# Optimization experiments

Measured on AMD Instinct MI355X. Metric: run time of the kernel, lower is better.

## Reference

```python
import jax, jax.numpy as jnp
import numpy as np

B, T, HW = 16, 64, 7
D = 768          # input_dim == base_dim
N = 12           # num_heads
C = D // N       # head_dim = 64
EPS = 1e-5


def layernorm(x, g, b):
    m = jnp.mean(x, axis=-1, keepdims=True)
    v = jnp.mean((x - m) ** 2, axis=-1, keepdims=True)
    return (x - m) * jax.lax.rsqrt(v + EPS) * g + b


def setup_inputs() -> dict:
    key = jax.random.key(0)
    ks = jax.random.split(key, 12)
    s = lambda k, shape: (jax.random.normal(k, shape, jnp.float32) * 0.02)
    return {
        "x": jax.random.normal(ks[0], (B, T, HW, HW, D), jnp.float32),
        "W_qkv": s(ks[1], (D, 3 * D)),                  # qkv_bias=False
        "Wpq": s(ks[2], (C, C, HW, HW)), "bpq": jnp.zeros((C,), jnp.float32),
        "Wpk": s(ks[3], (C, C, HW, HW)), "bpk": jnp.zeros((C,), jnp.float32),
        "Wpv": s(ks[4], (C, C, HW, HW)), "bpv": jnp.zeros((C,), jnp.float32),
        "g_q": jnp.ones((C,), jnp.float32), "be_q": jnp.zeros((C,), jnp.float32),
        "g_k": jnp.ones((C,), jnp.float32), "be_k": jnp.zeros((C,), jnp.float32),
        "g_v": jnp.ones((C,), jnp.float32), "be_v": jnp.zeros((C,), jnp.float32),
        "rel_pos_t": s(ks[5], (2 * T - 1, C)),          # (127, 64): matches dt, no interp
        "W_proj": s(ks[6], (D, D)), "b_proj": jnp.zeros((D,), jnp.float32),
    }


def reference(x, W_qkv, Wpq, bpq, Wpk, bpk, Wpv, bpv,
              g_q, be_q, g_k, be_k, g_v, be_v, rel_pos_t, W_proj, b_proj):
    b, t = x.shape[0], x.shape[1]
    # qkv projection -> (B,T,H,W,3,N,C)
    qkv = (x @ W_qkv).reshape(b, t, HW, HW, 3, N, C)
    q3, k3, v3 = qkv[..., 0, :, :], qkv[..., 1, :, :], qkv[..., 2, :, :]  # (B,T,H,W,N,C)
    # Conv3d kernel (1,7,7) on full 7x7 spatial == contraction over (h,w,c_in)
    q = jnp.einsum('bthwnc,dchw->bntd', q3, Wpq) + bpq   # (B,N,T,C)
    k = jnp.einsum('bthwnc,dchw->bntd', k3, Wpk) + bpk
    v = jnp.einsum('bthwnc,dchw->bntd', v3, Wpv) + bpv
    q = layernorm(q, g_q, be_q)
    k = layernorm(k, g_k, be_k)
    v = layernorm(v, g_v, be_v)
    scale = C ** -0.5
    attn = jnp.einsum('bntc,bnsc->bnts', q * scale, k)   # (B,N,T,T)
    # relative temporal position bias: gather table rows by distance, matmul with q
    dist = jnp.arange(t)[:, None] - jnp.arange(t)[None, :] + (t - 1)  # (T,T) in [0,2T-2]
    Rt = rel_pos_t[dist]                                  # (T,T,C)
    rel = jnp.einsum('bntc,tsc->bnts', q, Rt)
    attn = jax.nn.softmax(attn + rel, axis=-1)
    out = jnp.einsum('bnts,bnsc->bntc', attn, v) + q      # residual add of q
    out = out.transpose(0, 2, 1, 3).reshape(b, t, N * C)  # (B,T,D)
    return out @ W_proj + b_proj
```

## Files before the change

### kernel.cpp

```cpp
#include <hip/hip_runtime.h>


typedef __attribute__((ext_vector_type(8))) short bf16x8;
typedef __attribute__((ext_vector_type(4))) float f32x4;

#define AS1U(p) ((const __attribute__((address_space(1))) unsigned int*)(p))
#define AS3U(p) ((__attribute__((address_space(3))) unsigned int*)(p))

__device__ __forceinline__ unsigned short cvt_bf16(float x) {
  union { float f; unsigned int u; } v; v.f = x;
  unsigned int r = v.u + 0x7fffu + ((v.u >> 16) & 1u);
  return (unsigned short)(r >> 16);
}
__device__ __forceinline__ float bf2f(unsigned short h) {
  union { unsigned int u; float f; } v; v.u = ((unsigned int)h) << 16;
  return v.f;
}

__device__ __forceinline__ void wg_barrier() {
  asm volatile("" ::: "memory");
  __builtin_amdgcn_s_barrier();
  asm volatile("" ::: "memory");
}

__global__ __launch_bounds__(256) void cvt_x_k(const float* __restrict__ src,
                                               unsigned short* __restrict__ dst, int n8) {
  int i = blockIdx.x * 256 + threadIdx.x;
  if (i >= n8) return;
  const float4* s = (const float4*)src + (size_t)i * 2;
  float4 a = s[0], b = s[1];
  ushort4 r0 = { cvt_bf16(a.x), cvt_bf16(a.y), cvt_bf16(a.z), cvt_bf16(a.w) };
  ushort4 r1 = { cvt_bf16(b.x), cvt_bf16(b.y), cvt_bf16(b.z), cvt_bf16(b.w) };
  ushort4* d = (ushort4*)dst + (size_t)i * 2;
  d[0] = r0; d[1] = r1;
}

__global__ __launch_bounds__(256) void transpose_cvt_k(const float* __restrict__ src,
                                                       unsigned short* __restrict__ dst) {
  __shared__ float tl[32][33];
  int k0 = blockIdx.x * 32, n0 = blockIdx.y * 32;
  int tx = threadIdx.x & 31, ty = threadIdx.x >> 5;
#pragma unroll
  for (int r = 0; r < 32; r += 8)
    tl[ty + r][tx] = src[(size_t)(k0 + ty + r) * 2304 + n0 + tx];
  __syncthreads();
#pragma unroll
  for (int r = 0; r < 32; r += 8)
    dst[(size_t)(n0 + ty + r) * 768 + k0 + tx] = cvt_bf16(tl[tx][ty + r]);
}

__global__ __launch_bounds__(256) void prep_cvt_k(
    const float* __restrict__ Wpq, const float* __restrict__ Wpk,
    const float* __restrict__ Wpv, const float* __restrict__ relp,
    unsigned short* __restrict__ WpTT, unsigned short* __restrict__ relb) {
  int bid = blockIdx.x;
  if (bid < 2400) {
    int p = bid / 800;
    const float* src = (p == 0) ? Wpq : (p == 1) ? Wpk : Wpv;
    unsigned short* dst = WpTT + (size_t)p * 204800;
    int o = (bid - p * 800) * 256 + threadIdx.x;
    if (o >= 204800) return;
    int c = o & 63, d = (o >> 6) & 63, hw = o >> 12;
    dst[o] = (hw < 49) ? cvt_bf16(src[d * 3136 + c * 49 + hw]) : (unsigned short)0;
  } else {
    int i = (bid - 2400) * 256 + threadIdx.x;
    relb[i] = (i < 8128) ? cvt_bf16(relp[i]) : (unsigned short)0;
  }
}

__global__ __launch_bounds__(256, 2) void gemm_qkv_128(
    const unsigned short* __restrict__ A, const unsigned short* __restrict__ Bt,
    unsigned short* __restrict__ Cb, int nb_off) {
  __shared__ unsigned short As[2][8192];
  __shared__ unsigned short Bs[2][8192];

  const int orig = blockIdx.x;
  const int xcd = orig & 7;
  const int slot = orig >> 3;
  const int mb = xcd * 49 + slot / 9;
  const int nb = slot % 9 + nb_off;
  const int m0 = mb * 128, n0 = nb * 128;
  const int K = 768;

  const int tid = threadIdx.x;
  const int wave = tid >> 6, lane = tid & 63;
  const int quad = lane >> 4, l16 = lane & 15;
  const int wr = wave >> 1, wc = wave & 1;
  const int x7 = l16 & 7;

  const int srow = tid >> 3;
  const int cs = (tid & 7) ^ (srow & 7);
  const unsigned short* Ag[4];
  const unsigned short* Bg[4];
#pragma unroll
  for (int l = 0; l < 4; ++l) {
    Ag[l] = A + (size_t)(m0 + l * 32 + srow) * K + cs * 8;
    Bg[l] = Bt + (size_t)(n0 + l * 32 + srow) * K + cs * 8;
  }
  const int ldst = wave * 512;

#define STAGE_A(buf, kt) do {                                                      \
    const int ko_ = (kt) * 64;                                                     \
    _Pragma("unroll")                                                              \
    for (int l_ = 0; l_ < 4; ++l_)                                                 \
      __builtin_amdgcn_global_load_lds(AS1U(Ag[l_] + ko_),                         \
          AS3U(&As[buf][l_ * 2048 + ldst]), 16, 0, 0);                             \
  } while (0)

#define STAGE_B(buf, kt) do {                                                      \
    const int ko_ = (kt) * 64;                                                     \
    _Pragma("unroll")                                                              \
    for (int l_ = 0; l_ < 4; ++l_)                                                 \
      __builtin_amdgcn_global_load_lds(AS1U(Bg[l_] + ko_),                         \
          AS3U(&Bs[buf][l_ * 2048 + ldst]), 16, 0, 0);                             \
  } while (0)

#define LDA(dst, buf, mi) do {                                                     \
    _Pragma("unroll")                                                              \
    for (int fi_ = 0; fi_ < 2; ++fi_) {                                            \
      const int row_ = wr * 64 + (mi) * 32 + fi_ * 16 + l16;                       \
      _Pragma("unroll")                                                            \
      for (int ks_ = 0; ks_ < 2; ++ks_)                                            \
        dst[fi_][ks_] = *(const bf16x8*)&As[buf][row_ * 64 +                       \
            (((ks_ * 4 + quad) ^ x7) * 8)];                                        \
    }                                                                              \
  } while (0)

#define LDB(dst, buf, nj) do {                                                     \
    _Pragma("unroll")                                                              \
    for (int fj_ = 0; fj_ < 2; ++fj_) {                                            \
      const int row_ = wc * 64 + (nj) * 32 + fj_ * 16 + l16;                       \
      _Pragma("unroll")                                                            \
      for (int ks_ = 0; ks_ < 2; ++ks_)                                            \
        dst[fj_][ks_] = *(const bf16x8*)&Bs[buf][row_ * 64 +                       \
            (((ks_ * 4 + quad) ^ x7) * 8)];                                        \
    }                                                                              \
  } while (0)

#define MFMAQ(a_, b_, mi, nj) do {                                                 \
    _Pragma("unroll")                                                              \
    for (int ks_ = 0; ks_ < 2; ++ks_)                                              \
      _Pragma("unroll")                                                            \
      for (int fi_ = 0; fi_ < 2; ++fi_)                                            \
        _Pragma("unroll")                                                          \
        for (int fj_ = 0; fj_ < 2; ++fj_)                                          \
          acc[(mi) * 2 + fi_][(nj) * 2 + fj_] =                                    \
              __builtin_amdgcn_mfma_f32_16x16x32_bf16(a_[fi_][ks_],                \
                  b_[fj_][ks_], acc[(mi) * 2 + fi_][(nj) * 2 + fj_], 0, 0, 0);     \
  } while (0)

#define ITER(cur, DO_STAGE, kt2, VMI) do {                                         \
    asm volatile("s_waitcnt vmcnt(" #VMI ")" ::: "memory");                        \
    wg_barrier();                                                                  \
                                                           \
    LDA(af0, cur, 0); LDB(bf0, cur, 0);                                            \
    wg_barrier();                                                                  \
    __builtin_amdgcn_s_setprio(1); MFMAQ(af0, bf0, 0, 0);                          \
    __builtin_amdgcn_s_setprio(0);                                                 \
    wg_barrier();                                                                  \
                                                           \
    LDB(bf1, cur, 1);                                                              \
    wg_barrier();                                                                  \
    __builtin_amdgcn_s_setprio(1); MFMAQ(af0, bf1, 0, 1);                          \
    __builtin_amdgcn_s_setprio(0);                                                 \
    wg_barrier();                                                                  \
           \
    LDA(af1, cur, 1);                                                              \
    if (DO_STAGE) STAGE_B(cur, kt2);                                               \
    wg_barrier();                                                                  \
    __builtin_amdgcn_s_setprio(1); MFMAQ(af1, bf0, 1, 0);                          \
    __builtin_amdgcn_s_setprio(0);                                                 \
    wg_barrier();                                                                  \
           \
    if (DO_STAGE) STAGE_A(cur, kt2);                                               \
    __builtin_amdgcn_s_setprio(1); MFMAQ(af1, bf1, 1, 1);                          \
    __builtin_amdgcn_s_setprio(0);                                                 \
    wg_barrier();                                                                  \
  } while (0)

  f32x4 acc[4][4];
#pragma unroll
  for (int i = 0; i < 4; ++i)
#pragma unroll
    for (int j = 0; j < 4; ++j) acc[i][j] = (f32x4){0.f, 0.f, 0.f, 0.f};
  bf16x8 af0[2][2], af1[2][2], bf0[2][2], bf1[2][2];

  STAGE_B(0, 0); STAGE_A(0, 0);
  STAGE_B(1, 1); STAGE_A(1, 1);

  for (int kt = 0; kt < 10; kt += 2) {
    ITER(0, true, kt + 2, 8);
    ITER(1, true, kt + 3, 8);
  }
  ITER(0, false, 0, 8);
  ITER(1, false, 0, 0);

#undef ITER
#undef MFMAQ
#undef LDB
#undef LDA
#undef STAGE_B
#undef STAGE_A

#pragma unroll
  for (int i = 0; i < 4; ++i)
#pragma unroll
    for (int j = 0; j < 4; ++j)
#pragma unroll
      for (int r = 0; r < 4; ++r) {
        int row = m0 + wr * 64 + i * 16 + quad * 4 + r;
        int col = n0 + wc * 64 + j * 16 + l16;
        Cb[(size_t)row * 2304 + col] = cvt_bf16(acc[i][j][r]);
      }
}

__global__ __launch_bounds__(256) void pool_ln_mfma_k(
    const unsigned short* __restrict__ qkvb, const unsigned short* __restrict__ WpTT,
    const float* __restrict__ bq, const float* __restrict__ bk, const float* __restrict__ bv,
    const float* __restrict__ gq, const float* __restrict__ gk, const float* __restrict__ gv,
    const float* __restrict__ beq, const float* __restrict__ bek, const float* __restrict__ bev,
    unsigned short* __restrict__ oq, unsigned short* __restrict__ ok_,
    unsigned short* __restrict__ ov) {
  __shared__ float smem_f[16384];
  __shared__ float mu_s[64], rs_s[64];
  unsigned short* AB = (unsigned short*)smem_f;
  float* Ln = smem_f;

  const int n = blockIdx.x, p = blockIdx.y, b = blockIdx.z;
  const int tid = threadIdx.x;
  const int wave = tid >> 6, lane = tid & 63;
  const int quad = lane >> 4, l16 = lane & 15;
  const int wm = (wave >> 1) * 32, wn = (wave & 1) * 32;

  const int lr = lane >> 4, lg = lane & 15;
  const size_t abase = ((size_t)b * 3136) * 2304 + (size_t)p * 768 + (size_t)n * 64;
  const unsigned short* WpB = WpTT + (size_t)p * 204800;

  const unsigned short* pA[4];
  const unsigned short* pB[4];
#pragma unroll
  for (int q = 0; q < 4; ++q) {
    int r = wave * 16 + q * 4 + lr;
    int g = lg ^ (r & 15);
    pA[q] = qkvb + abase + (size_t)r * 112896 + (size_t)(g >> 3) * 2304 + (g & 7) * 8;
    pB[q] = WpB + (size_t)(g >> 3) * 4096 + r * 64 + (g & 7) * 8;
  }

#define PSTAGE(buf, it) do {                                                       \
    const size_t offA_ = (size_t)(it) * 4608;                                      \
    const size_t offB_ = (size_t)(it) * 8192;                                      \
    unsigned short* Ad_ = AB + (buf) * 8192;                                       \
    unsigned short* Bd_ = AB + 16384 + (buf) * 8192;                               \
    _Pragma("unroll")                                                              \
    for (int q_ = 0; q_ < 4; ++q_) {                                               \
      __builtin_amdgcn_global_load_lds(AS1U(pA[q_] + offA_),                       \
          AS3U(&Ad_[(wave * 16 + q_ * 4) * 128]), 16, 0, 0);                       \
      __builtin_amdgcn_global_load_lds(AS1U(pB[q_] + offB_),                       \
          AS3U(&Bd_[(wave * 16 + q_ * 4) * 128]), 16, 0, 0);                       \
    }                                                                              \
  } while (0)

#define PCOMPUTE(buf) do {                                                         \
    const unsigned short* Ad_ = AB + (buf) * 8192;                                 \
    const unsigned short* Bd_ = AB + 16384 + (buf) * 8192;                         \
    bf16x8 af_[2][4], bf_[2][4];                                                   \
    _Pragma("unroll")                                                              \
    for (int f_ = 0; f_ < 2; ++f_) {                                               \
      int ra_ = wm + f_ * 16 + l16;                                                \
      int rb_ = wn + f_ * 16 + l16;                                                \
      _Pragma("unroll")                                                            \
      for (int ki_ = 0; ki_ < 4; ++ki_) {                                          \
        af_[f_][ki_] = *(const bf16x8*)&Ad_[ra_ * 128 +                            \
            (((ki_ * 4 + quad) ^ (ra_ & 15)) * 8)];                                \
        bf_[f_][ki_] = *(const bf16x8*)&Bd_[rb_ * 128 +                            \
            (((ki_ * 4 + quad) ^ (rb_ & 15)) * 8)];                                \
      }                                                                            \
    }                                                                              \
    _Pragma("unroll")                                                              \
    for (int ki_ = 0; ki_ < 4; ++ki_)                                              \
      _Pragma("unroll")                                                            \
      for (int i_ = 0; i_ < 2; ++i_)                                               \
        _Pragma("unroll")                                                          \
        for (int j_ = 0; j_ < 2; ++j_)                                             \
          acc[i_][j_] = __builtin_amdgcn_mfma_f32_16x16x32_bf16(                   \
              af_[i_][ki_], bf_[j_][ki_], acc[i_][j_], 0, 0, 0);                   \
  } while (0)

  f32x4 acc[2][2];
#pragma unroll
  for (int i = 0; i < 2; ++i)
#pragma unroll
    for (int j = 0; j < 2; ++j) acc[i][j] = (f32x4){0.f, 0.f, 0.f, 0.f};

  PSTAGE(0, 0);
  for (int it2 = 0; it2 < 24; it2 += 2) {
    PSTAGE(1, it2 + 1);
    asm volatile("s_waitcnt vmcnt(8)" ::: "memory");
    wg_barrier();
    PCOMPUTE(0);
    wg_barrier();
    PSTAGE(0, it2 + 2);
    asm volatile("s_waitcnt vmcnt(8)" ::: "memory");
    wg_barrier();
    PCOMPUTE(1);
    wg_barrier();
  }
  asm volatile("s_waitcnt vmcnt(0)" ::: "memory");
  wg_barrier();
  PCOMPUTE(0);
  __syncthreads();

#undef PCOMPUTE
#undef PSTAGE

  const float* bias = (p == 0) ? bq : (p == 1) ? bk : bv;
  const float* g    = (p == 0) ? gq : (p == 1) ? gk : gv;
  const float* be   = (p == 0) ? beq : (p == 1) ? bek : bev;
  unsigned short* outp = (p == 0) ? oq : (p == 1) ? ok_ : ov;

#pragma unroll
  for (int i = 0; i < 2; ++i)
#pragma unroll
    for (int j = 0; j < 2; ++j)
#pragma unroll
      for (int r = 0; r < 4; ++r) {
        int t = wm + i * 16 + quad * 4 + r;
        int d = wn + j * 16 + l16;
        Ln[t * 65 + d] = acc[i][j][r] + bias[d];
      }
  __syncthreads();
  if (tid < 64) {
    float s = 0.f;
#pragma unroll 8
    for (int c = 0; c < 64; ++c) s += Ln[tid * 65 + c];
    float m = s * (1.f / 64.f);
    float v2 = 0.f;
#pragma unroll 8
    for (int c = 0; c < 64; ++c) { float dl = Ln[tid * 65 + c] - m; v2 += dl * dl; }
    mu_s[tid] = m;
    rs_s[tid] = rsqrtf(v2 * (1.f / 64.f) + 1e-5f);
  }
  __syncthreads();
  {
    int t = tid >> 2, d0 = (tid & 3) * 16;
    float m = mu_s[t], rv = rs_s[t];
    unsigned short ob[16];
#pragma unroll
    for (int j = 0; j < 16; ++j)
      ob[j] = cvt_bf16((Ln[t * 65 + d0 + j] - m) * rv * g[d0 + j] + be[d0 + j]);
    unsigned short* dst = outp + ((size_t)(b * 12 + n) * 64 + t) * 64 + d0;
    *(uint4*)dst = *(uint4*)ob;
    *(uint4*)(dst + 8) = *(uint4*)(ob + 8);
  }
}

__global__ __launch_bounds__(256) void attn_mfma_k(
    const unsigned short* __restrict__ qp, const unsigned short* __restrict__ kp,
    const unsigned short* __restrict__ vp, const unsigned short* __restrict__ relb,
    float* __restrict__ aout) {
  __shared__ unsigned short qs[64 * 64];
  __shared__ unsigned short ks[64 * 64];
  __shared__ unsigned short vt[64 * 64];
  __shared__ unsigned short rs[128 * 64];
  __shared__ float Gs[64 * 128];
  __shared__ unsigned short Ps[64 * 64];

  const int n = blockIdx.x, b = blockIdx.y;
  const int tid = threadIdx.x;
  const size_t base = ((size_t)b * 12 + n) * 4096;

  for (int i = tid; i < 512; i += 256) {
    ((uint4*)qs)[i] = ((const uint4*)(qp + base))[i];
    ((uint4*)ks)[i] = ((const uint4*)(kp + base))[i];
  }
  for (int i = tid; i < 1024; i += 256)
    ((uint4*)rs)[i] = ((const uint4*)relb)[i];
  {
    int s = tid >> 2, c0 = (tid & 3) * 16;
    unsigned short tmp[16];
    *(uint4*)tmp = *(const uint4*)(vp + base + s * 64 + c0);
    *(uint4*)(tmp + 8) = *(const uint4*)(vp + base + s * 64 + c0 + 8);
#pragma unroll
    for (int i = 0; i < 16; ++i) vt[(c0 + i) * 64 + s] = tmp[i];
  }
  __syncthreads();

  const int wave = tid >> 6, lane = tid & 63;
  const int quad = lane >> 4, l16 = lane & 15;
  const int tm = wave * 16;

  bf16x8 aq[2];
  aq[0] = *(const bf16x8*)&qs[(tm + l16) * 64 + quad * 8];
  aq[1] = *(const bf16x8*)&qs[(tm + l16) * 64 + quad * 8 + 32];

  f32x4 accqk[4], accg[8];
#pragma unroll
  for (int j = 0; j < 4; ++j) accqk[j] = (f32x4){0.f, 0.f, 0.f, 0.f};
#pragma unroll
  for (int j = 0; j < 8; ++j) accg[j] = (f32x4){0.f, 0.f, 0.f, 0.f};

#pragma unroll
  for (int ki = 0; ki < 2; ++ki) {
#pragma unroll
    for (int j = 0; j < 4; ++j) {
      bf16x8 bk = *(const bf16x8*)&ks[(j * 16 + l16) * 64 + quad * 8 + ki * 32];
      accqk[j] = __builtin_amdgcn_mfma_f32_16x16x32_bf16(aq[ki], bk, accqk[j], 0, 0, 0);
    }
#pragma unroll
    for (int j = 0; j < 8; ++j) {
      bf16x8 br = *(const bf16x8*)&rs[(j * 16 + l16) * 64 + quad * 8 + ki * 32];
      accg[j] = __builtin_amdgcn_mfma_f32_16x16x32_bf16(aq[ki], br, accg[j], 0, 0, 0);
    }
  }
#pragma unroll
  for (int j = 0; j < 8; ++j)
#pragma unroll
    for (int r = 0; r < 4; ++r)
      Gs[(tm + quad * 4 + r) * 128 + j * 16 + l16] = accg[j][r];
  __syncthreads();

#pragma unroll
  for (int r = 0; r < 4; ++r) {
    int t = tm + quad * 4 + r;
    float sv[4];
#pragma unroll
    for (int j = 0; j < 4; ++j) {
      int s = j * 16 + l16;
      sv[j] = 0.125f * accqk[j][r] + Gs[t * 128 + (t + 63 - s)];
    }
    float m = fmaxf(fmaxf(sv[0], sv[1]), fmaxf(sv[2], sv[3]));
    m = fmaxf(m, __shfl_xor(m, 1));
    m = fmaxf(m, __shfl_xor(m, 2));
    m = fmaxf(m, __shfl_xor(m, 4));
    m = fmaxf(m, __shfl_xor(m, 8));
    float e[4], sum = 0.f;
#pragma unroll
    for (int j = 0; j < 4; ++j) { e[j] = __expf(sv[j] - m); sum += e[j]; }
    sum += __shfl_xor(sum, 1);
    sum += __shfl_xor(sum, 2);
    sum += __shfl_xor(sum, 4);
    sum += __shfl_xor(sum, 8);
    float inv = 1.f / sum;
#pragma unroll
    for (int j = 0; j < 4; ++j)
      Ps[t * 64 + j * 16 + l16] = cvt_bf16(e[j] * inv);
  }
  __syncthreads();

  bf16x8 ap[2];
  ap[0] = *(const bf16x8*)&Ps[(tm + l16) * 64 + quad * 8];
  ap[1] = *(const bf16x8*)&Ps[(tm + l16) * 64 + quad * 8 + 32];
  f32x4 acco[4];
#pragma unroll
  for (int j = 0; j < 4; ++j) acco[j] = (f32x4){0.f, 0.f, 0.f, 0.f};
#pragma unroll
  for (int ki = 0; ki < 2; ++ki)
#pragma unroll
    for (int j = 0; j < 4; ++j) {
      bf16x8 bv = *(const bf16x8*)&vt[(j * 16 + l16) * 64 + quad * 8 + ki * 32];
      acco[j] = __builtin_amdgcn_mfma_f32_16x16x32_bf16(ap[ki], bv, acco[j], 0, 0, 0);
    }
#pragma unroll
  for (int j = 0; j < 4; ++j)
#pragma unroll
    for (int r = 0; r < 4; ++r) {
      int t = tm + quad * 4 + r;
      int c = j * 16 + l16;
      float o = acco[j][r] + bf2f(qs[t * 64 + c]);
      aout[((size_t)b * 64 + t) * 768 + n * 64 + c] = o;
    }
}

__global__ __launch_bounds__(256) void gemm_f32_k(
    const float* __restrict__ A, const float* __restrict__ Bm,
    const float* __restrict__ bias, float* __restrict__ Cm,
    int M, int Nn, int K) {
  __shared__ float As[16][68];
  __shared__ float Bs[16][64];
  const int tid = threadIdx.x;
  const int ty = tid >> 4, tx = tid & 15;
  const int m0 = blockIdx.y * 64, n0 = blockIdx.x * 64;

  const int la_m = tid >> 2;
  const int la_k = (tid & 3) << 2;
  const int lb_k = tid >> 4;
  const int lb_n = (tid & 15) << 2;

  const float* Ap = A + (size_t)(m0 + la_m) * K + la_k;
  const float* Bp = Bm + (size_t)lb_k * Nn + n0 + lb_n;

  float acc[4][4];
#pragma unroll
  for (int i = 0; i < 4; ++i)
#pragma unroll
    for (int j = 0; j < 4; ++j) acc[i][j] = 0.f;

  for (int k0 = 0; k0 < K; k0 += 16) {
    float4 av = *(const float4*)(Ap + k0);
    float4 bv = *(const float4*)(Bp + (size_t)k0 * Nn);
    As[la_k + 0][la_m] = av.x;
    As[la_k + 1][la_m] = av.y;
    As[la_k + 2][la_m] = av.z;
    As[la_k + 3][la_m] = av.w;
    *(float4*)&Bs[lb_k][lb_n] = bv;
    __syncthreads();
#pragma unroll
    for (int kk = 0; kk < 16; ++kk) {
      float af[4], bf[4];
      *(float4*)af = *(const float4*)&As[kk][ty << 2];
      *(float4*)bf = *(const float4*)&Bs[kk][tx << 2];
#pragma unroll
      for (int i = 0; i < 4; ++i)
#pragma unroll
        for (int j = 0; j < 4; ++j) acc[i][j] += af[i] * bf[j];
    }
    __syncthreads();
  }

  float bb[4] = {0.f, 0.f, 0.f, 0.f};
  if (bias) {
#pragma unroll
    for (int j = 0; j < 4; ++j) bb[j] = bias[n0 + (tx << 2) + j];
  }
#pragma unroll
  for (int i = 0; i < 4; ++i) {
    float4 o;
    o.x = acc[i][0] + bb[0];
    o.y = acc[i][1] + bb[1];
    o.z = acc[i][2] + bb[2];
    o.w = acc[i][3] + bb[3];
    *(float4*)(Cm + (size_t)(m0 + (ty << 2) + i) * Nn + n0 + (tx << 2)) = o;
  }
}

extern "C" void kernel_launch(void* const* d_in, const int* in_sizes, int n_in,
                              void* d_out, int out_size, void* d_ws, size_t ws_size,
                              hipStream_t stream) {
  const float* x     = (const float*)d_in[0];
  const float* Wqkv  = (const float*)d_in[1];
  const float* Wpq   = (const float*)d_in[2];
  const float* bpq   = (const float*)d_in[3];
  const float* Wpk   = (const float*)d_in[4];
  const float* bpk   = (const float*)d_in[5];
  const float* Wpv   = (const float*)d_in[6];
  const float* bpv   = (const float*)d_in[7];
  const float* gq    = (const float*)d_in[8];
  const float* beq   = (const float*)d_in[9];
  const float* gk    = (const float*)d_in[10];
  const float* bek   = (const float*)d_in[11];
  const float* gv    = (const float*)d_in[12];
  const float* bev   = (const float*)d_in[13];
  const float* relp  = (const float*)d_in[14];
  const float* Wproj = (const float*)d_in[15];
  const float* bproj = (const float*)d_in[16];
  float* out = (float*)d_out;

  unsigned short* u = (unsigned short*)d_ws;
  unsigned short* xbf   = u;
  unsigned short* qkvbf = u + 38535168ull;
  unsigned short* WqkvT = u + 154140672ull;
  unsigned short* WpTT  = u + 155910144ull;
  unsigned short* relb  = u + 156524544ull;
  unsigned short* qpb   = u + 156532736ull;
  unsigned short* kpb   = u + 157319168ull;
  unsigned short* vpb   = u + 158105600ull;
  float* aout = (float*)(u + 158892032ull);

  cvt_x_k<<<18816, 256, 0, stream>>>(x, xbf, 4816896);
  transpose_cvt_k<<<dim3(24, 72), 256, 0, stream>>>(Wqkv, WqkvT);
  prep_cvt_k<<<2432, 256, 0, stream>>>(Wpq, Wpk, Wpv, relp, WpTT, relb);

  gemm_qkv_128<<<3528, 256, 0, stream>>>(xbf, WqkvT, qkvbf, 0);
  gemm_qkv_128<<<3528, 256, 0, stream>>>(xbf, WqkvT, qkvbf, 9);

  pool_ln_mfma_k<<<dim3(12, 3, 16), 256, 0, stream>>>(
      qkvbf, WpTT, bpq, bpk, bpv, gq, gk, gv, beq, bek, bev, qpb, kpb, vpb);

  attn_mfma_k<<<dim3(12, 16), 256, 0, stream>>>(qpb, kpb, vpb, relb, aout);

  gemm_f32_k<<<dim3(12, 16), 256, 0, stream>>>(aout, Wproj, bproj, out, 1024, 768, 768);
}
```

Before: 594.3 us.

## Fuse fp32-to-bf16 conversion of x into QKV GEMM A-tile staging

Removes the separate cvt_x_k pass. The QKV GEMM now reads fp32 x directly into registers, converts it to bf16 and writes it to LDS, instead of using global_load_lds on a pre-converted buffer. This saves one full read of x plus the write and re-read of the bf16 copy. In exchange, the A operand is read as fp32 (twice the bytes) by each of the two GEMM launches, and register pressure and VALU conversion work rise inside the pipelined loop, with reworked waitcnt and barrier placement.

```diff
diff --git a/kernel.cpp b/kernel.cpp
--- a/kernel.cpp
+++ b/kernel.cpp
@@ -21,18 +21,6 @@
   asm volatile("" ::: "memory");
   __builtin_amdgcn_s_barrier();
   asm volatile("" ::: "memory");
-}
-
-__global__ __launch_bounds__(256) void cvt_x_k(const float* __restrict__ src,
-                                               unsigned short* __restrict__ dst, int n8) {
-  int i = blockIdx.x * 256 + threadIdx.x;
-  if (i >= n8) return;
-  const float4* s = (const float4*)src + (size_t)i * 2;
-  float4 a = s[0], b = s[1];
-  ushort4 r0 = { cvt_bf16(a.x), cvt_bf16(a.y), cvt_bf16(a.z), cvt_bf16(a.w) };
-  ushort4 r1 = { cvt_bf16(b.x), cvt_bf16(b.y), cvt_bf16(b.z), cvt_bf16(b.w) };
-  ushort4* d = (ushort4*)dst + (size_t)i * 2;
-  d[0] = r0; d[1] = r1;
 }
 
 __global__ __launch_bounds__(256) void transpose_cvt_k(const float* __restrict__ src,
@@ -69,7 +57,7 @@
 }
 
 __global__ __launch_bounds__(256, 2) void gemm_qkv_128(
-    const unsigned short* __restrict__ A, const unsigned short* __restrict__ Bt,
+    const float* __restrict__ X, const unsigned short* __restrict__ Bt,
     unsigned short* __restrict__ Cb, int nb_off) {
   __shared__ unsigned short As[2][8192];
   __shared__ unsigned short Bs[2][8192];
@@ -90,21 +78,35 @@
 
   const int srow = tid >> 3;
   const int cs = (tid & 7) ^ (srow & 7);
-  const unsigned short* Ag[4];
+  const float* Xg[4];
   const unsigned short* Bg[4];
 #pragma unroll
   for (int l = 0; l < 4; ++l) {
-    Ag[l] = A + (size_t)(m0 + l * 32 + srow) * K + cs * 8;
+    Xg[l] = X + (size_t)(m0 + l * 32 + srow) * K + cs * 8;
     Bg[l] = Bt + (size_t)(n0 + l * 32 + srow) * K + cs * 8;
   }
-  const int ldst = wave * 512;
-
-#define STAGE_A(buf, kt) do {                                                      \
+
+  float4 xr[8];
+
+#define STAGE_A_LOAD(kt) do {                                                      \
     const int ko_ = (kt) * 64;                                                     \
     _Pragma("unroll")                                                              \
-    for (int l_ = 0; l_ < 4; ++l_)                                                 \
-      __builtin_amdgcn_global_load_lds(AS1U(Ag[l_] + ko_),                         \
-          AS3U(&As[buf][l_ * 2048 + ldst]), 16, 0, 0);                             \
+    for (int l_ = 0; l_ < 4; ++l_) {                                               \
+      xr[2 * l_]     = *(const float4*)(Xg[l_] + ko_);                             \
+      xr[2 * l_ + 1] = *(const float4*)(Xg[l_] + ko_ + 4);                         \
+    }                                                                              \
+  } while (0)
+
+#define STAGE_A_WRITE(buf) do {                                                    \
+    _Pragma("unroll")                                                              \
+    for (int l_ = 0; l_ < 4; ++l_) {                                               \
+      unsigned short o_[8];                                                        \
+      o_[0] = cvt_bf16(xr[2 * l_].x);     o_[1] = cvt_bf16(xr[2 * l_].y);          \
+      o_[2] = cvt_bf16(xr[2 * l_].z);     o_[3] = cvt_bf16(xr[2 * l_].w);          \
+      o_[4] = cvt_bf16(xr[2 * l_ + 1].x); o_[5] = cvt_bf16(xr[2 * l_ + 1].y);      \
+      o_[6] = cvt_bf16(xr[2 * l_ + 1].z); o_[7] = cvt_bf16(xr[2 * l_ + 1].w);      \
+      *(uint4*)&As[buf][l_ * 2048 + tid * 8] = *(const uint4*)o_;                  \
+    }                                                                              \
   } while (0)
 
 #define STAGE_B(buf, kt) do {                                                      \
@@ -112,7 +114,7 @@
     _Pragma("unroll")                                                              \
     for (int l_ = 0; l_ < 4; ++l_)                                                 \
       __builtin_amdgcn_global_load_lds(AS1U(Bg[l_] + ko_),                         \
-          AS3U(&Bs[buf][l_ * 2048 + ldst]), 16, 0, 0);                             \
+          AS3U(&Bs[buf][l_ * 2048 + wave * 512]), 16, 0, 0);                       \
   } while (0)
 
 #define LDA(dst, buf, mi) do {                                                     \
@@ -149,11 +151,10 @@
                   b_[fj_][ks_], acc[(mi) * 2 + fi_][(nj) * 2 + fj_], 0, 0, 0);     \
   } while (0)
 
-#define ITER(cur, DO_STAGE, kt2, VMI) do {                                         \
-    asm volatile("s_waitcnt vmcnt(" #VMI ")" ::: "memory");                        \
-    wg_barrier();                                                                  \
-                                                           \
+#define ITER(cur, DO_STAGE, kt2, VMI4) do {                                        \
+                   \
     LDA(af0, cur, 0); LDB(bf0, cur, 0);                                            \
+    if (DO_STAGE) STAGE_A_LOAD(kt2);                                               \
     wg_barrier();                                                                  \
     __builtin_amdgcn_s_setprio(1); MFMAQ(af0, bf0, 0, 0);                          \
     __builtin_amdgcn_s_setprio(0);                                                 \
@@ -164,17 +165,19 @@
     __builtin_amdgcn_s_setprio(1); MFMAQ(af0, bf1, 0, 1);                          \
     __builtin_amdgcn_s_setprio(0);                                                 \
     wg_barrier();                                                                  \
-           \
+                   \
     LDA(af1, cur, 1);                                                              \
     if (DO_STAGE) STAGE_B(cur, kt2);                                               \
     wg_barrier();                                                                  \
     __builtin_amdgcn_s_setprio(1); MFMAQ(af1, bf0, 1, 0);                          \
     __builtin_amdgcn_s_setprio(0);                                                 \
     wg_barrier();                                                                  \
-           \
-    if (DO_STAGE) STAGE_A(cur, kt2);                                               \
+             \
+    asm volatile("s_waitcnt vmcnt(" #VMI4 ")" ::: "memory");                       \
+    if (DO_STAGE) STAGE_A_WRITE(cur);                                              \
     __builtin_amdgcn_s_setprio(1); MFMAQ(af1, bf1, 1, 1);                          \
     __builtin_amdgcn_s_setprio(0);                                                 \
+    asm volatile("s_waitcnt lgkmcnt(0)" ::: "memory");                             \
     wg_barrier();                                                                  \
   } while (0)
 
@@ -185,14 +188,22 @@
     for (int j = 0; j < 4; ++j) acc[i][j] = (f32x4){0.f, 0.f, 0.f, 0.f};
   bf16x8 af0[2][2], af1[2][2], bf0[2][2], bf1[2][2];
 
-  STAGE_B(0, 0); STAGE_A(0, 0);
-  STAGE_B(1, 1); STAGE_A(1, 1);
+  STAGE_A_LOAD(0);
+  STAGE_B(0, 0);
+  asm volatile("s_waitcnt vmcnt(4)" ::: "memory");
+  STAGE_A_WRITE(0);
+  STAGE_A_LOAD(1);
+  STAGE_B(1, 1);
+  asm volatile("s_waitcnt vmcnt(4)" ::: "memory");
+  STAGE_A_WRITE(1);
+  asm volatile("s_waitcnt lgkmcnt(0)" ::: "memory");
+  wg_barrier();
 
   for (int kt = 0; kt < 10; kt += 2) {
-    ITER(0, true, kt + 2, 8);
-    ITER(1, true, kt + 3, 8);
-  }
-  ITER(0, false, 0, 8);
+    ITER(0, true, kt + 2, 4);
+    ITER(1, true, kt + 3, 4);
+  }
+  ITER(0, false, 0, 0);
   ITER(1, false, 0, 0);
 
 #undef ITER
@@ -200,7 +211,8 @@
 #undef LDB
 #undef LDA
 #undef STAGE_B
-#undef STAGE_A
+#undef STAGE_A_WRITE
+#undef STAGE_A_LOAD
 
 #pragma unroll
   for (int i = 0; i < 4; ++i)
@@ -556,7 +568,6 @@
   float* out = (float*)d_out;
 
   unsigned short* u = (unsigned short*)d_ws;
-  unsigned short* xbf   = u;
   unsigned short* qkvbf = u + 38535168ull;
   unsigned short* WqkvT = u + 154140672ull;
   unsigned short* WpTT  = u + 155910144ull;
@@ -566,12 +577,11 @@
   unsigned short* vpb   = u + 158105600ull;
   float* aout = (float*)(u + 158892032ull);
 
-  cvt_x_k<<<18816, 256, 0, stream>>>(x, xbf, 4816896);
   transpose_cvt_k<<<dim3(24, 72), 256, 0, stream>>>(Wqkv, WqkvT);
   prep_cvt_k<<<2432, 256, 0, stream>>>(Wpq, Wpk, Wpv, relp, WpTT, relb);
 
-  gemm_qkv_128<<<3528, 256, 0, stream>>>(xbf, WqkvT, qkvbf, 0);
-  gemm_qkv_128<<<3528, 256, 0, stream>>>(xbf, WqkvT, qkvbf, 9);
+  gemm_qkv_128<<<3528, 256, 0, stream>>>(x, WqkvT, qkvbf, 0);
+  gemm_qkv_128<<<3528, 256, 0, stream>>>(x, WqkvT, qkvbf, 9);
 
   pool_ln_mfma_k<<<dim3(12, 3, 16), 256, 0, stream>>>(
       qkvbf, WpTT, bpq, bpk, bpv, gq, gk, gv, beq, bek, bev, qpb, kpb, vpb);
```

After: 682.9 us. 1.15x slower.
